# Optimization experiments

Hardware: AMD Instinct MI355X
Metric: run time of the kernel (lower is better)

The kernel has to match this reference:

```python
import jax, jax.numpy as jnp
import numpy as np

LRELU_SLOPE = 0.2  # PyG GATConv default negative_slope
LN_EPS = 1e-5


def _layer_norm(x, g, b):
    mu = x.mean(-1, keepdims=True)
    var = x.var(-1, keepdims=True)
    return (x - mu) / jnp.sqrt(var + LN_EPS) * g + b


def _gat_conv(x, src, dst, W, a_src, a_dst, bias, heads, out_c, concat):
    # PyG GATConv (eval mode, self-loops already appended to src/dst).
    N = x.shape[0]
    h = (x @ W).reshape(N, heads, out_c)            # [N,H,C]
    e_src = (h * a_src).sum(-1)                     # [N,H]
    e_dst = (h * a_dst).sum(-1)                     # [N,H]
    e = jax.nn.leaky_relu(e_src[src] + e_dst[dst], LRELU_SLOPE)  # [E,H]
    # segment softmax over incoming edges of each dst node
    m = jax.ops.segment_max(e, dst, num_segments=N)
    m = jnp.where(jnp.isfinite(m), m, 0.0)
    w = jnp.exp(e - m[dst])
    denom = jax.ops.segment_sum(w, dst, num_segments=N)
    alpha = w / (denom[dst] + 1e-16)                # [E,H]
    out = jax.ops.segment_sum(h[src] * alpha[:, :, None], dst, num_segments=N)  # [N,H,C]
    out = out.reshape(N, heads * out_c) if concat else out.mean(1)
    return out + bias


def setup_inputs() -> dict:
    key = jax.random.key(0)
    ks = jax.random.split(key, 16)
    N, E, F0, Hd, H, G = 50000, 800000, 32, 32, 4, 512
    s = 0.1
    nrm = lambda k, shape: jax.random.normal(k, shape, jnp.float32) * s
    d = {}
    d['x'] = jax.random.normal(ks[0], (N, F0), jnp.float32)
    d['edge_index'] = jax.random.randint(ks[1], (2, E), 0, N)
    d['batch'] = jnp.sort(jax.random.randint(ks[2], (N,), 0, G))
    d['num_graphs'] = G
    # layer 1: F0 -> (Hd, H heads, concat)
    d['W1'] = nrm(ks[3], (F0, H * Hd)); d['as1'] = nrm(ks[4], (H, Hd)); d['ad1'] = nrm(ks[5], (H, Hd))
    d['b1'] = jnp.zeros((H * Hd,)); d['g1'] = jnp.ones((H * Hd,)); d['be1'] = jnp.zeros((H * Hd,))
    # layer 2: H*Hd -> (Hd, H heads, concat)
    d['W2'] = nrm(ks[6], (H * Hd, H * Hd)); d['as2'] = nrm(ks[7], (H, Hd)); d['ad2'] = nrm(ks[8], (H, Hd))
    d['b2'] = jnp.zeros((H * Hd,)); d['g2'] = jnp.ones((H * Hd,)); d['be2'] = jnp.zeros((H * Hd,))
    # layer 3: H*Hd -> (Hd, 1 head, mean)
    d['W3'] = nrm(ks[9], (H * Hd, Hd)); d['as3'] = nrm(ks[10], (1, Hd)); d['ad3'] = nrm(ks[11], (1, Hd))
    d['b3'] = jnp.zeros((Hd,)); d['g3'] = jnp.ones((Hd,)); d['be3'] = jnp.zeros((Hd,))
    # classifier MLP: 2*Hd -> Hd -> Hd//2 -> 1 (torch Linear [out,in])
    d['cW1'] = nrm(ks[12], (Hd, 2 * Hd)); d['cb1'] = jnp.zeros((Hd,))
    d['cW2'] = nrm(ks[13], (Hd // 2, Hd)); d['cb2'] = jnp.zeros((Hd // 2,))
    d['cW3'] = nrm(ks[14], (1, Hd // 2)); d['cb3'] = jnp.zeros((1,))
    return d


def reference(x, edge_index, batch, num_graphs,
              W1, as1, ad1, b1, g1, be1,
              W2, as2, ad2, b2, g2, be2,
              W3, as3, ad3, b3, g3, be3,
              cW1, cb1, cW2, cb2, cW3, cb3):
    N = x.shape[0]
    loop = jnp.arange(N)
    src = jnp.concatenate([edge_index[0], loop])
    dst = jnp.concatenate([edge_index[1], loop])
    h = jax.nn.elu(_layer_norm(_gat_conv(x, src, dst, W1, as1, ad1, b1, 4, 32, True), g1, be1))
    h = jax.nn.elu(_layer_norm(_gat_conv(h, src, dst, W2, as2, ad2, b2, 4, 32, True), g2, be2))
    h = jax.nn.elu(_layer_norm(_gat_conv(h, src, dst, W3, as3, ad3, b3, 1, 32, False), g3, be3))
    cnt = jax.ops.segment_sum(jnp.ones((N,), h.dtype), batch, num_segments=num_graphs)
    x_mean = jax.ops.segment_sum(h, batch, num_segments=num_graphs) / jnp.maximum(cnt, 1.0)[:, None]
    x_max = jax.ops.segment_max(h, batch, num_segments=num_graphs)
    f = jnp.concatenate([x_mean, x_max], axis=1)        # [G, 64]
    f = jax.nn.relu(f @ cW1.T + cb1)
    f = jax.nn.relu(f @ cW2.T + cb2)
    return (f @ cW3.T + cb3).squeeze(-1)                 # [G]
```

## Files before the change

kernel.cpp:

```cpp
#include <hip/hip_runtime.h>
#include <hip/hip_fp16.h>
#include <math.h>

#define CDIV(a, b) (((a) + (b) - 1) / (b))
#define SCAN_BS 1024
#define NBUK 512
#define ATILE 4096

typedef _Float16 f16x8 __attribute__((ext_vector_type(8)));
typedef float f32x4 __attribute__((ext_vector_type(4)));

__device__ __forceinline__ unsigned encf(float v) {
    unsigned u = __float_as_uint(v);
    return (u & 0x80000000u) ? ~u : (u | 0x80000000u);
}
__device__ __forceinline__ float decf(unsigned k) {
    unsigned u = (k & 0x80000000u) ? (k ^ 0x80000000u) : ~k;
    return __uint_as_float(u);
}

__device__ __forceinline__ float lrelu(float v) {
    return v > 0.f ? v : 0.2f * v;
}

__global__ __launch_bounds__(256) void gemm_kernel(
    const float* __restrict__ X, const float* __restrict__ W,
    float* __restrict__ Y, int M, int K, int Nout) {
    int idx = blockIdx.x * blockDim.x + threadIdx.x;
    if (idx >= M * Nout) return;
    int row = idx / Nout;
    int col = idx - row * Nout;
    const float* xr = X + (size_t)row * K;
    const float* wc = W + col;
    float acc = 0.f;
    for (int k = 0; k < K; k += 4) {
        float4 xv = *(const float4*)(xr + k);
        acc += xv.x * wc[(size_t)(k + 0) * Nout];
        acc += xv.y * wc[(size_t)(k + 1) * Nout];
        acc += xv.z * wc[(size_t)(k + 2) * Nout];
        acc += xv.w * wc[(size_t)(k + 3) * Nout];
    }
    Y[idx] = acc;
}

__device__ __forceinline__ void wprep_one(const float* __restrict__ W,
                                          __half* __restrict__ Whf, int K,
                                          int NOUT, int idx) {
    int NK = K / 32;
    int l = idx & 63, f = idx >> 6;
    int ks = f % NK, tt = f / NK;
    int quad = l >> 4, c15 = l & 15;
    _Float16 v[8];
#pragma unroll
    for (int j = 0; j < 8; ++j) {
        int k = ks * 32 + quad * 8 + j;
        int n = tt * 16 + c15;
        v[j] = (_Float16)W[(size_t)k * NOUT + n];
    }
    *(uint4*)(Whf + (size_t)idx * 8) = *(uint4*)v;
}

__global__ __launch_bounds__(256) void wprep_all_kernel(
    const float* __restrict__ W1, const float* __restrict__ W2,
    const float* __restrict__ W3, __half* __restrict__ wh1,
    __half* __restrict__ wh2, __half* __restrict__ wh3,
    int* __restrict__ rowptr, int N, int E) {
    int idx = blockIdx.x * 256 + threadIdx.x;
    if (idx == 0) rowptr[N] = E + N;
    if (idx < 512) {
        wprep_one(W1, wh1, 32, 128, idx);
    } else if (idx < 2560) {
        wprep_one(W2, wh2, 128, 128, idx - 512);
    } else if (idx < 3072) {
        wprep_one(W3, wh3, 128, 32, idx - 2560);
    }
}

__device__ __forceinline__ f16x8 loadA(const float* p) {
    float4 lo = *(const float4*)p;
    float4 hi = *(const float4*)(p + 4);
    f16x8 a;
    a[0] = (_Float16)lo.x; a[1] = (_Float16)lo.y;
    a[2] = (_Float16)lo.z; a[3] = (_Float16)lo.w;
    a[4] = (_Float16)hi.x; a[5] = (_Float16)hi.y;
    a[6] = (_Float16)hi.z; a[7] = (_Float16)hi.w;
    return a;
}
__device__ __forceinline__ f16x8 loadA(const __half* p) {
    return *(const f16x8*)p;
}

template <int K, int NOUT, int HH, typename XT>
__global__ __launch_bounds__(256) void gemm_mfma_attn(
    const XT* __restrict__ X, const __half* __restrict__ Whf,
    __half* __restrict__ Y, const float* __restrict__ a_src,
    const float* __restrict__ a_dst, float* __restrict__ es,
    float* __restrict__ ed, int M) {
    constexpr int NK = K / 32, NT = NOUT / 16;
    static_assert(NT == 2 * HH, "32 channels per head assumed");
    int wave = threadIdx.x >> 6, lane = threadIdx.x & 63;
    int quad = lane >> 4, c15 = lane & 15;
    int row0 = (blockIdx.x * 4 + wave) * 16;
    if (row0 >= M) return;
    int arow = row0 + c15;
    if (arow >= M) arow = M - 1;
    const XT* xr = X + (size_t)arow * K + quad * 8;
    const f16x8* bp = (const f16x8*)Whf;
    f32x4 acc[NT];
#pragma unroll
    for (int t = 0; t < NT; ++t) {
        acc[t][0] = 0.f; acc[t][1] = 0.f; acc[t][2] = 0.f; acc[t][3] = 0.f;
    }
#pragma unroll
    for (int ks = 0; ks < NK; ++ks) {
        f16x8 a = loadA(xr + ks * 32);
#pragma unroll
        for (int t = 0; t < NT; ++t) {
            f16x8 b = bp[(t * NK + ks) * 64 + lane];
            acc[t] = __builtin_amdgcn_mfma_f32_16x16x32_f16(a, b, acc[t],
                                                            0, 0, 0);
        }
    }
#pragma unroll
    for (int r = 0; r < 4; ++r) {
        int row = row0 + quad * 4 + r;
        if (row < M) {
#pragma unroll
            for (int t = 0; t < NT; ++t)
                Y[(size_t)row * NOUT + t * 16 + c15] = (__half)acc[t][r];
        }
    }
    float asv[NT], adv[NT];
#pragma unroll
    for (int t = 0; t < NT; ++t) {
        asv[t] = a_src[t * 16 + c15];
        adv[t] = a_dst[t * 16 + c15];
    }
#pragma unroll
    for (int h = 0; h < HH; ++h) {
#pragma unroll
        for (int r = 0; r < 4; ++r) {
            float s = acc[2 * h][r] * asv[2 * h] +
                      acc[2 * h + 1][r] * asv[2 * h + 1];
            float dd = acc[2 * h][r] * adv[2 * h] +
                       acc[2 * h + 1][r] * adv[2 * h + 1];
#pragma unroll
            for (int off = 8; off >= 1; off >>= 1) {
                s += __shfl_xor(s, off);
                dd += __shfl_xor(dd, off);
            }
            int row = row0 + quad * 4 + r;
            if (row < M) {
                if (c15 == 0) es[row * HH + h] = s;
                if (c15 == 1) ed[row * HH + h] = dd;
            }
        }
    }
}

__global__ __launch_bounds__(256) void binA1_kernel(
    const int* __restrict__ ei, int E, int* __restrict__ ghist,
    int* __restrict__ pool0, int poolN) {
    __shared__ int lh[NBUK];
    int t = threadIdx.x;
    int gid = blockIdx.x * 256 + t;
    if (gid < poolN) pool0[gid] = 0;
    for (int i = t; i < NBUK; i += 256) lh[i] = 0;
    __syncthreads();
    int base = blockIdx.x * ATILE;
#pragma unroll 4
    for (int j = 0; j < ATILE / 256; ++j) {
        int idx = base + t + 256 * j;
        if (idx < E) atomicAdd(&lh[ei[E + idx] >> 7], 1);
    }
    __syncthreads();
    int* gh = ghist + (size_t)blockIdx.x * NBUK;
    for (int i = t; i < NBUK; i += 256) gh[i] = lh[i];
}

__global__ __launch_bounds__(64) void binA2a_kernel(
    int* __restrict__ ghist, int* __restrict__ tot, int nblk) {
    int b = blockIdx.x;
    int lane = threadIdx.x;
    int accb = 0;
    for (int chunk = 0; chunk < nblk; chunk += 64) {
        int i = chunk + lane;
        int v = (i < nblk) ? ghist[(size_t)i * NBUK + b] : 0;
        int s = v;
        for (int off = 1; off < 64; off <<= 1) {
            int tv = __shfl_up(s, off);
            if (lane >= off) s += tv;
        }
        if (i < nblk) ghist[(size_t)i * NBUK + b] = s - v + accb;
        accb += __shfl(s, 63);
    }
    if (lane == 0) tot[b] = accb;
}

__device__ __forceinline__ void bucketScan(const int* __restrict__ tot,
                                           int* __restrict__ sc, int t,
                                           int& a0, int& a1, int& excl) {
    a0 = tot[2 * t];
    a1 = tot[2 * t + 1];
    int pair = a0 + a1;
    sc[t] = pair;
    __syncthreads();
#pragma unroll
    for (int off = 1; off < 256; off <<= 1) {
        int v = (t >= off) ? sc[t - off] : 0;
        __syncthreads();
        sc[t] += v;
        __syncthreads();
    }
    excl = sc[t] - pair;
}

__global__ __launch_bounds__(256) void binA3_kernel(
    const int* __restrict__ ei, int E, const int* __restrict__ ghist,
    const int* __restrict__ tot, unsigned* __restrict__ ebuf) {
    __shared__ int lcur[NBUK];
    __shared__ int sc[256];
    int t = threadIdx.x;
    int a0, a1, excl;
    bucketScan(tot, sc, t, a0, a1, excl);
    const int* gh = ghist + (size_t)blockIdx.x * NBUK;
    lcur[2 * t] = gh[2 * t] + excl;
    lcur[2 * t + 1] = gh[2 * t + 1] + excl + a0;
    __syncthreads();
    int base = blockIdx.x * ATILE;
#pragma unroll 4
    for (int j = 0; j < ATILE / 256; ++j) {
        int idx = base + t + 256 * j;
        if (idx < E) {
            int s = ei[idx];
            int d = ei[E + idx];
            int pos = atomicAdd(&lcur[d >> 7], 1);
            ebuf[pos] = ((unsigned)d << 16) | (unsigned)s;
        }
    }
}

__global__ __launch_bounds__(256) void binB_kernel(
    const unsigned* __restrict__ ebuf, const int* __restrict__ tot,
    int* __restrict__ rowptr, int* __restrict__ csrc, int N) {
    __shared__ int cnt_[128];
    __shared__ int pre[128];
    __shared__ int lcur[128];
    __shared__ int sc[256];
    __shared__ int begS;
    int b = blockIdx.x;
    int t = threadIdx.x;
    int n0 = b << 7;
    int totb = tot[b];
    if (t < 128) cnt_[t] = 0;
    int a0, a1, excl;
    bucketScan(tot, sc, t, a0, a1, excl);
    if (t == (b >> 1)) begS = (b & 1) ? (excl + a0) : excl;
    __syncthreads();
    int beg = begS, end = begS + totb;
    for (int i = beg + t; i < end; i += 256)
        atomicAdd(&cnt_[(ebuf[i] >> 16) - n0], 1);
    __syncthreads();
    if (t < 128) pre[t] = (n0 + t < N) ? (cnt_[t] + 1) : 0;
    __syncthreads();
    for (int off = 1; off < 128; off <<= 1) {
        int v = 0;
        if (t < 128 && t >= off) v = pre[t - off];
        __syncthreads();
        if (t < 128) pre[t] += v;
        __syncthreads();
    }
    int cbase = beg + n0;
    if (t < 128 && n0 + t < N) {
        int ex = pre[t] - (cnt_[t] + 1);
        int rp = cbase + ex;
        rowptr[n0 + t] = rp;
        csrc[rp] = n0 + t;
        lcur[t] = rp + 1;
    }
    __syncthreads();
    for (int i = beg + t; i < end; i += 256) {
        unsigned e = ebuf[i];
        int d = (int)(e >> 16) - n0;
        int s = (int)(e & 0xFFFFu);
        int pos = atomicAdd(&lcur[d], 1);
        csrc[pos] = s;
    }
}

__global__ __launch_bounds__(256) void attn_kernel(
    const float* __restrict__ h, const float* __restrict__ a_src,
    const float* __restrict__ a_dst, float* __restrict__ es,
    float* __restrict__ ed, int N, int H, int C) {
    int idx = blockIdx.x * blockDim.x + threadIdx.x;
    if (idx >= N * H) return;
    int n = idx / H;
    int hh = idx - n * H;
    const float* hp = h + (size_t)n * H * C + (size_t)hh * C;
    const float* ap = a_src + hh * C;
    const float* bp = a_dst + hh * C;
    float s = 0.f, d = 0.f;
    for (int c = 0; c < C; c += 4) {
        float4 hv = *(const float4*)(hp + c);
        float4 av = *(const float4*)(ap + c);
        float4 bv = *(const float4*)(bp + c);
        s += hv.x * av.x + hv.y * av.y + hv.z * av.z + hv.w * av.w;
        d += hv.x * bv.x + hv.y * bv.y + hv.z * bv.z + hv.w * bv.w;
    }
    es[idx] = s;
    ed[idx] = d;
}

__global__ __launch_bounds__(256) void deg_kernel(const int* __restrict__ ei,
                                                  int E,
                                                  int* __restrict__ deg) {
    int e = blockIdx.x * blockDim.x + threadIdx.x;
    if (e >= E) return;
    atomicAdd(&deg[ei[E + e]], 1);
}

__global__ __launch_bounds__(SCAN_BS) void scan1_kernel(
    const int* __restrict__ deg, int* __restrict__ rowptr,
    int* __restrict__ bsum, int N) {
    __shared__ int tmp[SCAN_BS];
    int tid = threadIdx.x;
    int gid = blockIdx.x * SCAN_BS + tid;
    int v = (gid < N) ? (deg[gid] + 1) : 0;
    tmp[tid] = v;
    __syncthreads();
    for (int off = 1; off < SCAN_BS; off <<= 1) {
        int t = (tid >= off) ? tmp[tid - off] : 0;
        __syncthreads();
        tmp[tid] += t;
        __syncthreads();
    }
    if (gid < N) rowptr[gid] = tmp[tid] - v;
    if (tid == SCAN_BS - 1) bsum[blockIdx.x] = tmp[tid];
}

__global__ void scan2_kernel(int* __restrict__ bsum, int nb) {
    if (threadIdx.x == 0 && blockIdx.x == 0) {
        int acc = 0;
        for (int i = 0; i < nb; ++i) {
            int t = bsum[i];
            bsum[i] = acc;
            acc += t;
        }
    }
}

__global__ __launch_bounds__(SCAN_BS) void scan3_kernel(
    int* __restrict__ rowptr, int* __restrict__ cursor,
    int* __restrict__ csrc, const int* __restrict__ bsum, int N, int total) {
    int gid = blockIdx.x * SCAN_BS + threadIdx.x;
    if (gid < N) {
        int v = rowptr[gid] + bsum[blockIdx.x];
        rowptr[gid] = v;
        cursor[gid] = v + 1;
        csrc[v] = gid;
    }
    if (gid == 0) rowptr[N] = total;
}

__global__ __launch_bounds__(256) void scatter_kernel(
    const int* __restrict__ ei, int E, int* __restrict__ cursor,
    int* __restrict__ csrc) {
    int e = blockIdx.x * blockDim.x + threadIdx.x;
    if (e >= E) return;
    int s = ei[e];
    int d = ei[E + e];
    int pos = atomicAdd(&cursor[d], 1);
    csrc[pos] = s;
}

__global__ __launch_bounds__(256) void aggr_ln128_kernel(
    const int* __restrict__ rowptr, const int* __restrict__ csrc,
    const __half* __restrict__ h, const float* __restrict__ es,
    const float* __restrict__ ed, const float* __restrict__ bias,
    const float* __restrict__ gam, const float* __restrict__ bet,
    __half* __restrict__ outp, int N) {
    constexpr int D = 128, H = 4;
    int wave = (blockIdx.x * blockDim.x + threadIdx.x) >> 6;
    int lane = threadIdx.x & 63;
    int grp = lane >> 5;
    int li = lane & 31;
    int d = wave * 2 + grp;
    if (d >= N) return;
    int c = li * 4;
    int hh = li >> 3;
    float edv = ed[d * H + hh];
    float l = 0.f;
    float ax = 0.f, ay = 0.f, az = 0.f, aw = 0.f;
    int k = rowptr[d], end = rowptr[d + 1];
    for (; k + 8 <= end; k += 8) {
        int s[8];
#pragma unroll
        for (int j = 0; j < 8; ++j) s[j] = csrc[k + j];
        float e[8];
#pragma unroll
        for (int j = 0; j < 8; ++j) e[j] = es[s[j] * H + hh];
        uint2 u[8];
#pragma unroll
        for (int j = 0; j < 8; ++j)
            u[j] = *(const uint2*)(h + (size_t)s[j] * D + c);
#pragma unroll
        for (int j = 0; j < 8; ++j) {
            float w = __expf(lrelu(e[j] + edv));
            float2 f0 = __half22float2(*(__half2*)&u[j].x);
            float2 f1 = __half22float2(*(__half2*)&u[j].y);
            l += w;
            ax += w * f0.x; ay += w * f0.y; az += w * f1.x; aw += w * f1.y;
        }
    }
    for (; k + 4 <= end; k += 4) {
        int s[4];
#pragma unroll
        for (int j = 0; j < 4; ++j) s[j] = csrc[k + j];
        float e[4];
#pragma unroll
        for (int j = 0; j < 4; ++j) e[j] = es[s[j] * H + hh];
        uint2 u[4];
#pragma unroll
        for (int j = 0; j < 4; ++j)
            u[j] = *(const uint2*)(h + (size_t)s[j] * D + c);
#pragma unroll
        for (int j = 0; j < 4; ++j) {
            float w = __expf(lrelu(e[j] + edv));
            float2 f0 = __half22float2(*(__half2*)&u[j].x);
            float2 f1 = __half22float2(*(__half2*)&u[j].y);
            l += w;
            ax += w * f0.x; ay += w * f0.y; az += w * f1.x; aw += w * f1.y;
        }
    }
    for (; k < end; ++k) {
        int s = csrc[k];
        float w = __expf(lrelu(es[s * H + hh] + edv));
        uint2 u = *(const uint2*)(h + (size_t)s * D + c);
        float2 f0 = __half22float2(*(__half2*)&u.x);
        float2 f1 = __half22float2(*(__half2*)&u.y);
        l += w;
        ax += w * f0.x; ay += w * f0.y; az += w * f1.x; aw += w * f1.y;
    }
    float rl = 1.f / (l + 1e-16f);
    float4 b4 = *(const float4*)(bias + c);
    float v0 = ax * rl + b4.x;
    float v1 = ay * rl + b4.y;
    float v2 = az * rl + b4.z;
    float v3 = aw * rl + b4.w;
    float s = v0 + v1 + v2 + v3;
    float ss = v0 * v0 + v1 * v1 + v2 * v2 + v3 * v3;
    for (int off = 16; off; off >>= 1) {
        s += __shfl_xor(s, off);
        ss += __shfl_xor(ss, off);
    }
    float mean = s / D;
    float var = ss / D - mean * mean;
    float rstd = rsqrtf(var + 1e-5f);
    float4 g4 = *(const float4*)(gam + c);
    float4 t4 = *(const float4*)(bet + c);
    float4 o;
    o.x = (v0 - mean) * rstd * g4.x + t4.x;
    o.y = (v1 - mean) * rstd * g4.y + t4.y;
    o.z = (v2 - mean) * rstd * g4.z + t4.z;
    o.w = (v3 - mean) * rstd * g4.w + t4.w;
    o.x = o.x > 0.f ? o.x : expm1f(o.x);
    o.y = o.y > 0.f ? o.y : expm1f(o.y);
    o.z = o.z > 0.f ? o.z : expm1f(o.z);
    o.w = o.w > 0.f ? o.w : expm1f(o.w);
    __half2 p0 = __floats2half2_rn(o.x, o.y);
    __half2 p1 = __floats2half2_rn(o.z, o.w);
    uint2 u;
    u.x = *(unsigned*)&p0;
    u.y = *(unsigned*)&p1;
    *(uint2*)(outp + (size_t)d * D + c) = u;
}

__global__ __launch_bounds__(256) void aggr_ln32_pool_kernel(
    const int* __restrict__ rowptr, const int* __restrict__ csrc,
    const __half* __restrict__ h, const float* __restrict__ es,
    const float* __restrict__ ed, const float* __restrict__ bias,
    const float* __restrict__ gam, const float* __restrict__ bet,
    const int* __restrict__ batch, float* __restrict__ psum,
    unsigned* __restrict__ pmax, float* __restrict__ cnt, int N) {
    constexpr int D = 32;
    __shared__ float lsum[2][32];
    __shared__ unsigned lmax[2][32];
    __shared__ float lcnt[2];
    __shared__ int g0s;
    int tid = threadIdx.x;
    int wave = (blockIdx.x * blockDim.x + tid) >> 6;
    int lane = tid & 63;
    int half = lane >> 5;
    int c = lane & 31;
    int d = wave * 2 + half;
    int dbase = blockIdx.x * 8;
    if (tid < 64) {
        lsum[tid >> 5][tid & 31] = 0.f;
        lmax[tid >> 5][tid & 31] = 0u;
    }
    if (tid < 2) lcnt[tid] = 0.f;
    if (tid == 0) g0s = batch[dbase < N ? dbase : (N - 1)];
    __syncthreads();
    int g0 = g0s;
    bool active = d < N;
    if (active) {
        float edv = ed[d];
        float l = 0.f, acc = 0.f;
        int k = rowptr[d], end = rowptr[d + 1];
        for (; k + 8 <= end; k += 8) {
            int s[8];
#pragma unroll
            for (int j = 0; j < 8; ++j) s[j] = csrc[k + j];
            float e[8];
#pragma unroll
            for (int j = 0; j < 8; ++j) e[j] = es[s[j]];
            float hv[8];
#pragma unroll
            for (int j = 0; j < 8; ++j)
                hv[j] = __half2float(h[(size_t)s[j] * D + c]);
#pragma unroll
            for (int j = 0; j < 8; ++j) {
                float w = __expf(lrelu(e[j] + edv));
                l += w;
                acc += w * hv[j];
            }
        }
        for (; k + 4 <= end; k += 4) {
            int s[4];
#pragma unroll
            for (int j = 0; j < 4; ++j) s[j] = csrc[k + j];
            float e[4];
#pragma unroll
            for (int j = 0; j < 4; ++j) e[j] = es[s[j]];
            float hv[4];
#pragma unroll
            for (int j = 0; j < 4; ++j)
                hv[j] = __half2float(h[(size_t)s[j] * D + c]);
#pragma unroll
            for (int j = 0; j < 4; ++j) {
                float w = __expf(lrelu(e[j] + edv));
                l += w;
                acc += w * hv[j];
            }
        }
        for (; k < end; ++k) {
            int s = csrc[k];
            float w = __expf(lrelu(es[s] + edv));
            l += w;
            acc += w * __half2float(h[(size_t)s * D + c]);
        }
        float v = acc / (l + 1e-16f) + bias[c];
        float sm = v, ss = v * v;
        for (int off = 16; off; off >>= 1) {
            sm += __shfl_xor(sm, off);
            ss += __shfl_xor(ss, off);
        }
        float mean = sm / D;
        float var = ss / D - mean * mean;
        float rstd = rsqrtf(var + 1e-5f);
        float o = (v - mean) * rstd * gam[c] + bet[c];
        o = o > 0.f ? o : expm1f(o);
        int g = batch[d];
        int goff = g - g0;
        if (goff >= 0 && goff < 2) {
            atomicAdd(&lsum[goff][c], o);
            atomicMax(&lmax[goff][c], encf(o));
            if (c == 0) atomicAdd(&lcnt[goff], 1.0f);
        } else {
            atomicAdd(&psum[g * D + c], o);
            atomicMax(&pmax[g * D + c], encf(o));
            if (c == 0) atomicAdd(&cnt[g], 1.0f);
        }
    }
    __syncthreads();
    if (tid < 64) {
        int go = tid >> 5, cc = tid & 31;
        unsigned m = lmax[go][cc];
        if (m != 0u) {
            int gg = g0 + go;
            atomicAdd(&psum[gg * D + cc], lsum[go][cc]);
            atomicMax(&pmax[gg * D + cc], m);
            if (cc == 0) atomicAdd(&cnt[gg], lcnt[go]);
        }
    }
}

__global__ __launch_bounds__(256) void aggr_csr_kernel(
    const int* __restrict__ rowptr, const int* __restrict__ csrc,
    const float* __restrict__ h, const float* __restrict__ es,
    const float* __restrict__ ed, float* __restrict__ outp, int N, int H,
    int C) {
    int D = H * C;
    int wave = (blockIdx.x * blockDim.x + threadIdx.x) >> 6;
    int lane = threadIdx.x & 63;
    if (wave >= N) return;
    int d = wave;
    int c0 = lane, c1 = lane + 64;
    bool a0 = c0 < D, a1 = c1 < D;
    int h0 = a0 ? c0 / C : 0;
    int h1 = a1 ? c1 / C : 0;
    float edv0 = a0 ? ed[d * H + h0] : 0.f;
    float edv1 = a1 ? ed[d * H + h1] : 0.f;
    float m0 = -INFINITY, m1 = -INFINITY;
    float l0 = 0.f, l1 = 0.f, acc0 = 0.f, acc1 = 0.f;
    int beg = rowptr[d], end = rowptr[d + 1];
    for (int k = beg; k < end; ++k) {
        int s = csrc[k];
        const float* hp = h + (size_t)s * D;
        if (a0) {
            float v = lrelu(es[s * H + h0] + edv0);
            float nm = fmaxf(m0, v);
            float sc = __expf(m0 - nm);
            float w = __expf(v - nm);
            l0 = l0 * sc + w;
            acc0 = acc0 * sc + w * hp[c0];
            m0 = nm;
        }
        if (a1) {
            float v = lrelu(es[s * H + h1] + edv1);
            float nm = fmaxf(m1, v);
            float sc = __expf(m1 - nm);
            float w = __expf(v - nm);
            l1 = l1 * sc + w;
            acc1 = acc1 * sc + w * hp[c1];
            m1 = nm;
        }
    }
    if (a0) outp[(size_t)d * D + c0] = acc0 / (l0 + 1e-16f);
    if (a1) outp[(size_t)d * D + c1] = acc1 / (l1 + 1e-16f);
}

__global__ __launch_bounds__(64) void ln_elu_kernel(
    const float* __restrict__ in, const float* __restrict__ bias,
    const float* __restrict__ gam, const float* __restrict__ bet,
    float* __restrict__ outp, int D) {
    int n = blockIdx.x;
    int lane = threadIdx.x;
    int c0 = lane, c1 = lane + 64;
    bool a0 = c0 < D, a1 = c1 < D;
    float v0 = 0.f, v1 = 0.f;
    if (a0) v0 = in[(size_t)n * D + c0] + bias[c0];
    if (a1) v1 = in[(size_t)n * D + c1] + bias[c1];
    float s = v0 + v1;
    float ss = v0 * v0 + v1 * v1;
    for (int off = 32; off; off >>= 1) {
        s += __shfl_xor(s, off);
        ss += __shfl_xor(ss, off);
    }
    float mean = s / D;
    float var = ss / D - mean * mean;
    float rstd = rsqrtf(var + 1e-5f);
    if (a0) {
        float o = (v0 - mean) * rstd * gam[c0] + bet[c0];
        outp[(size_t)n * D + c0] = o > 0.f ? o : expm1f(o);
    }
    if (a1) {
        float o = (v1 - mean) * rstd * gam[c1] + bet[c1];
        outp[(size_t)n * D + c1] = o > 0.f ? o : expm1f(o);
    }
}

__global__ __launch_bounds__(256) void pool_kernel(
    const float* __restrict__ h, const int* __restrict__ batch, int N, int C,
    float* __restrict__ psum, unsigned* __restrict__ pmax,
    float* __restrict__ cnt) {
    int idx = blockIdx.x * blockDim.x + threadIdx.x;
    if (idx >= N * C) return;
    int n = idx / C;
    int c = idx - n * C;
    int g = batch[n];
    float v = h[(size_t)n * C + c];
    atomicAdd(&psum[g * C + c], v);
    atomicMax(&pmax[g * C + c], encf(v));
    if (c == 0) atomicAdd(&cnt[g], 1.0f);
}

__global__ __launch_bounds__(64) void mlp_kernel(
    const float* __restrict__ psum, const unsigned* __restrict__ pmax,
    const float* __restrict__ cnt, const float* __restrict__ cW1,
    const float* __restrict__ cb1, const float* __restrict__ cW2,
    const float* __restrict__ cb2, const float* __restrict__ cW3,
    const float* __restrict__ cb3, float* __restrict__ outp, int C) {
    __shared__ float f[64];
    __shared__ float t1[32];
    __shared__ float t2[16];
    int g = blockIdx.x;
    int t = threadIdx.x;
    float c = fmaxf(cnt[g], 1.0f);
    if (t < C) {
        f[t] = psum[g * C + t] / c;
    } else if (t < 2 * C) {
        unsigned k = pmax[g * C + (t - C)];
        f[t] = (k == 0u) ? -INFINITY : decf(k);
    }
    __syncthreads();
    if (t < 32) {
        float a = cb1[t];
        for (int i = 0; i < 64; ++i) a += f[i] * cW1[t * 64 + i];
        t1[t] = fmaxf(a, 0.f);
    }
    __syncthreads();
    if (t < 16) {
        float a = cb2[t];
        for (int i = 0; i < 32; ++i) a += t1[i] * cW2[t * 32 + i];
        t2[t] = fmaxf(a, 0.f);
    }
    __syncthreads();
    if (t == 0) {
        float a = cb3[0];
        for (int i = 0; i < 16; ++i) a += t2[i] * cW3[i];
        outp[g] = a;
    }
}

extern "C" void kernel_launch(void* const* d_in, const int* in_sizes, int n_in,
                              void* d_out, int out_size, void* d_ws,
                              size_t ws_size, hipStream_t stream) {
    const float* x = (const float*)d_in[0];
    const int* ei = (const int*)d_in[1];
    const int* batch = (const int*)d_in[2];
    const float* W1 = (const float*)d_in[4];
    const float* as1 = (const float*)d_in[5];
    const float* ad1 = (const float*)d_in[6];
    const float* b1 = (const float*)d_in[7];
    const float* g1 = (const float*)d_in[8];
    const float* be1 = (const float*)d_in[9];
    const float* W2 = (const float*)d_in[10];
    const float* as2 = (const float*)d_in[11];
    const float* ad2 = (const float*)d_in[12];
    const float* b2 = (const float*)d_in[13];
    const float* g2 = (const float*)d_in[14];
    const float* be2 = (const float*)d_in[15];
    const float* W3 = (const float*)d_in[16];
    const float* as3 = (const float*)d_in[17];
    const float* ad3 = (const float*)d_in[18];
    const float* b3 = (const float*)d_in[19];
    const float* g3 = (const float*)d_in[20];
    const float* be3 = (const float*)d_in[21];
    const float* cW1 = (const float*)d_in[22];
    const float* cb1 = (const float*)d_in[23];
    const float* cW2 = (const float*)d_in[24];
    const float* cb2 = (const float*)d_in[25];
    const float* cW3 = (const float*)d_in[26];
    const float* cb3 = (const float*)d_in[27];

    const int N = in_sizes[2];
    const int E = in_sizes[1] / 2;
    const int F0 = in_sizes[0] / N;
    const int Hd = in_sizes[19];
    const int H = in_sizes[5] / Hd;
    const int D = H * Hd;
    const int H3 = in_sizes[17] / Hd;
    const int G = out_size;
    const int EN = E + N;
    const bool shapes_ok = (F0 == 32 && Hd == 32 && H == 4 && D == 128 &&
                            H3 == 1 && N <= 65536);

    char* w = (char*)d_ws;
    size_t off = 0;
    auto carve = [&](size_t bytes) -> void* {
        void* p = w + off;
        off = (off + bytes + 255) & ~(size_t)255;
        return p;
    };
    float* Q = (float*)carve((size_t)N * D * 4);
    __half* Qh = (__half*)Q;
    float* R = (float*)carve((size_t)N * D * 4);
    float* P = (float*)carve((size_t)N * D * 4);
    __half* Ph = (__half*)P;
    float* es = (float*)carve((size_t)N * H * 4);
    float* ed = (float*)carve((size_t)N * H * 4);
    int* rowptr = (int*)carve((size_t)(N + 1) * 4);
    int* cursor = (int*)carve((size_t)N * 4);
    int* csrc = (int*)carve((size_t)EN * 4);
    int* bsum = (int*)carve((size_t)CDIV(N, SCAN_BS) * 4);
    const int nblkA = CDIV(E, ATILE);
    int* ghist = (int*)carve((size_t)nblkA * NBUK * 4);
    int* tot = (int*)carve((size_t)NBUK * 4);
    unsigned* ebuf = (unsigned*)carve((size_t)E * 4);
    __half* wh1 = (__half*)carve((size_t)8 * 1 * 64 * 8 * 2);
    __half* wh2 = (__half*)carve((size_t)8 * 4 * 64 * 8 * 2);
    __half* wh3 = (__half*)carve((size_t)2 * 4 * 64 * 8 * 2);
    float* psum = (float*)carve((size_t)G * Hd * 4);
    unsigned* pmax = (unsigned*)carve((size_t)G * Hd * 4);
    float* cnt = (float*)carve((size_t)G * 4);
    (void)ws_size;
    (void)n_in;

    const int BLK = 256;
    const int nb = CDIV(N, SCAN_BS);
    const int poolInts = G * Hd * 2 + G;

    if (shapes_ok) {
        binA1_kernel<<<nblkA, 256, 0, stream>>>(ei, E, ghist, (int*)psum,
                                                poolInts);
        binA2a_kernel<<<NBUK, 64, 0, stream>>>(ghist, tot, nblkA);
        binA3_kernel<<<nblkA, 256, 0, stream>>>(ei, E, ghist, tot, ebuf);
        binB_kernel<<<CDIV(N, 128), 256, 0, stream>>>(ebuf, tot, rowptr,
                                                      csrc, N);
        wprep_all_kernel<<<12, 256, 0, stream>>>(W1, W2, W3, wh1, wh2, wh3,
                                                 rowptr, N, E);
        gemm_mfma_attn<32, 128, 4, float><<<CDIV(N, 64), 256, 0, stream>>>(
            x, wh1, Qh, as1, ad1, es, ed, N);
        aggr_ln128_kernel<<<CDIV(N, 8), 256, 0, stream>>>(
            rowptr, csrc, Qh, es, ed, b1, g1, be1, Ph, N);
        gemm_mfma_attn<128, 128, 4, __half><<<CDIV(N, 64), 256, 0, stream>>>(
            Ph, wh2, Qh, as2, ad2, es, ed, N);
        aggr_ln128_kernel<<<CDIV(N, 8), 256, 0, stream>>>(
            rowptr, csrc, Qh, es, ed, b2, g2, be2, Ph, N);
        gemm_mfma_attn<128, 32, 1, __half><<<CDIV(N, 64), 256, 0, stream>>>(
            Ph, wh3, Qh, as3, ad3, es, ed, N);
        aggr_ln32_pool_kernel<<<CDIV(N, 8), 256, 0, stream>>>(
            rowptr, csrc, Qh, es, ed, b3, g3, be3, batch, psum, pmax, cnt, N);
    } else {
        hipMemsetAsync(psum, 0, (size_t)G * Hd * 4, stream);
        hipMemsetAsync(pmax, 0, (size_t)G * Hd * 4, stream);
        hipMemsetAsync(cnt, 0, (size_t)G * 4, stream);
        hipMemsetAsync(cursor, 0, (size_t)N * 4, stream);
        deg_kernel<<<CDIV(E, BLK), BLK, 0, stream>>>(ei, E, cursor);
        scan1_kernel<<<nb, SCAN_BS, 0, stream>>>(cursor, rowptr, bsum, N);
        scan2_kernel<<<1, 64, 0, stream>>>(bsum, nb);
        scan3_kernel<<<nb, SCAN_BS, 0, stream>>>(rowptr, cursor, csrc, bsum, N, EN);
        scatter_kernel<<<CDIV(E, BLK), BLK, 0, stream>>>(ei, E, cursor, csrc);
        gemm_kernel<<<CDIV(N * D, BLK), BLK, 0, stream>>>(x, W1, Q, N, F0, D);
        attn_kernel<<<CDIV(N * H, BLK), BLK, 0, stream>>>(Q, as1, ad1, es, ed, N, H, Hd);
        aggr_csr_kernel<<<CDIV(N, 4), BLK, 0, stream>>>(rowptr, csrc, Q, es, ed, R, N, H, Hd);
        ln_elu_kernel<<<N, 64, 0, stream>>>(R, b1, g1, be1, P, D);
        gemm_kernel<<<CDIV(N * D, BLK), BLK, 0, stream>>>(P, W2, Q, N, D, D);
        attn_kernel<<<CDIV(N * H, BLK), BLK, 0, stream>>>(Q, as2, ad2, es, ed, N, H, Hd);
        aggr_csr_kernel<<<CDIV(N, 4), BLK, 0, stream>>>(rowptr, csrc, Q, es, ed, R, N, H, Hd);
        ln_elu_kernel<<<N, 64, 0, stream>>>(R, b2, g2, be2, P, D);
        gemm_kernel<<<CDIV(N * Hd, BLK), BLK, 0, stream>>>(P, W3, Q, N, D, Hd);
        attn_kernel<<<CDIV(N * H3, BLK), BLK, 0, stream>>>(Q, as3, ad3, es, ed, N, H3, Hd);
        aggr_csr_kernel<<<CDIV(N, 4), BLK, 0, stream>>>(rowptr, csrc, Q, es, ed, R, N, H3, Hd);
        ln_elu_kernel<<<N, 64, 0, stream>>>(R, b3, g3, be3, P, Hd);
        pool_kernel<<<CDIV(N * Hd, BLK), BLK, 0, stream>>>(P, batch, N, Hd, psum, pmax, cnt);
    }

    mlp_kernel<<<G, 64, 0, stream>>>(psum, pmax, cnt, cW1, cb1, cW2, cb2, cW3,
                                     cb3, (float*)d_out, Hd);
}
```

Before: 295.4 us.

## Assign one wavefront per destination node and split edges across lane subgroups

The GAT aggregation kernels now map one 64-lane wavefront to each destination node instead of two nodes per wave. Lanes are split into subgroups that each process a different incoming edge: four groups of 16 lanes with 16-byte loads for the 128-wide layers, and eight groups of 8 lanes with 8-byte loads for the 32-wide layer. Partial sums are combined with cross-lane shuffles. The aim is more memory-level parallelism per node and wider gathers, at the cost of extra shuffle reductions, idle lanes during the LayerNorm/ELU epilogue, and twice as many blocks.

```diff
diff --git a/kernel.cpp b/kernel.cpp
--- a/kernel.cpp
+++ b/kernel.cpp
@@ -380,99 +380,109 @@
     const float* __restrict__ gam, const float* __restrict__ bet,
     __half* __restrict__ outp, int N) {
     constexpr int D = 128, H = 4;
-    int wave = (blockIdx.x * blockDim.x + threadIdx.x) >> 6;
+    int d = (blockIdx.x * blockDim.x + threadIdx.x) >> 6;
     int lane = threadIdx.x & 63;
-    int grp = lane >> 5;
-    int li = lane & 31;
-    int d = wave * 2 + grp;
     if (d >= N) return;
-    int c = li * 4;
-    int hh = li >> 3;
+    int sub = lane >> 4;
+    int cl = lane & 15;
+    int c = cl * 8;
+    int hh = cl >> 2;
     float edv = ed[d * H + hh];
+    float acc[8];
+#pragma unroll
+    for (int i = 0; i < 8; ++i) acc[i] = 0.f;
     float l = 0.f;
-    float ax = 0.f, ay = 0.f, az = 0.f, aw = 0.f;
-    int k = rowptr[d], end = rowptr[d + 1];
-    for (; k + 8 <= end; k += 8) {
-        int s[8];
-#pragma unroll
-        for (int j = 0; j < 8; ++j) s[j] = csrc[k + j];
-        float e[8];
-#pragma unroll
-        for (int j = 0; j < 8; ++j) e[j] = es[s[j] * H + hh];
-        uint2 u[8];
-#pragma unroll
-        for (int j = 0; j < 8; ++j)
-            u[j] = *(const uint2*)(h + (size_t)s[j] * D + c);
-#pragma unroll
-        for (int j = 0; j < 8; ++j) {
-            float w = __expf(lrelu(e[j] + edv));
-            float2 f0 = __half22float2(*(__half2*)&u[j].x);
-            float2 f1 = __half22float2(*(__half2*)&u[j].y);
+    int beg = rowptr[d], end = rowptr[d + 1];
+    int k = beg;
+    for (; k + 16 <= end; k += 16) {
+        int s[4];
+#pragma unroll
+        for (int r = 0; r < 4; ++r) s[r] = csrc[k + 4 * r + sub];
+        float e[4];
+#pragma unroll
+        for (int r = 0; r < 4; ++r) e[r] = es[s[r] * H + hh];
+        uint4 u[4];
+#pragma unroll
+        for (int r = 0; r < 4; ++r)
+            u[r] = *(const uint4*)(h + (size_t)s[r] * D + c);
+#pragma unroll
+        for (int r = 0; r < 4; ++r) {
+            float w = __expf(lrelu(e[r] + edv));
             l += w;
-            ax += w * f0.x; ay += w * f0.y; az += w * f1.x; aw += w * f1.y;
-        }
-    }
-    for (; k + 4 <= end; k += 4) {
-        int s[4];
-#pragma unroll
-        for (int j = 0; j < 4; ++j) s[j] = csrc[k + j];
-        float e[4];
-#pragma unroll
-        for (int j = 0; j < 4; ++j) e[j] = es[s[j] * H + hh];
-        uint2 u[4];
-#pragma unroll
-        for (int j = 0; j < 4; ++j)
-            u[j] = *(const uint2*)(h + (size_t)s[j] * D + c);
-#pragma unroll
-        for (int j = 0; j < 4; ++j) {
-            float w = __expf(lrelu(e[j] + edv));
-            float2 f0 = __half22float2(*(__half2*)&u[j].x);
-            float2 f1 = __half22float2(*(__half2*)&u[j].y);
-            l += w;
-            ax += w * f0.x; ay += w * f0.y; az += w * f1.x; aw += w * f1.y;
-        }
-    }
-    for (; k < end; ++k) {
-        int s = csrc[k];
-        float w = __expf(lrelu(es[s * H + hh] + edv));
-        uint2 u = *(const uint2*)(h + (size_t)s * D + c);
-        float2 f0 = __half22float2(*(__half2*)&u.x);
-        float2 f1 = __half22float2(*(__half2*)&u.y);
+            const __half2* hp = (const __half2*)&u[r];
+#pragma unroll
+            for (int i = 0; i < 4; ++i) {
+                float2 f = __half22float2(hp[i]);
+                acc[2 * i] += w * f.x;
+                acc[2 * i + 1] += w * f.y;
+            }
+        }
+    }
+    for (; k < end; k += 4) {
+        int slot = k + sub;
+        bool ok = slot < end;
+        int s = csrc[ok ? slot : beg];
+        float e = es[s * H + hh];
+        uint4 u = *(const uint4*)(h + (size_t)s * D + c);
+        float w = ok ? __expf(lrelu(e + edv)) : 0.f;
         l += w;
-        ax += w * f0.x; ay += w * f0.y; az += w * f1.x; aw += w * f1.y;
-    }
+        const __half2* hp = (const __half2*)&u;
+#pragma unroll
+        for (int i = 0; i < 4; ++i) {
+            float2 f = __half22float2(hp[i]);
+            acc[2 * i] += w * f.x;
+            acc[2 * i + 1] += w * f.y;
+        }
+    }
+#pragma unroll
+    for (int i = 0; i < 8; ++i) acc[i] += __shfl_xor(acc[i], 16);
+    l += __shfl_xor(l, 16);
+#pragma unroll
+    for (int i = 0; i < 8; ++i) acc[i] += __shfl_xor(acc[i], 32);
+    l += __shfl_xor(l, 32);
     float rl = 1.f / (l + 1e-16f);
-    float4 b4 = *(const float4*)(bias + c);
-    float v0 = ax * rl + b4.x;
-    float v1 = ay * rl + b4.y;
-    float v2 = az * rl + b4.z;
-    float v3 = aw * rl + b4.w;
-    float s = v0 + v1 + v2 + v3;
-    float ss = v0 * v0 + v1 * v1 + v2 * v2 + v3 * v3;
-    for (int off = 16; off; off >>= 1) {
-        s += __shfl_xor(s, off);
-        ss += __shfl_xor(ss, off);
-    }
-    float mean = s / D;
-    float var = ss / D - mean * mean;
+    float4 b0 = *(const float4*)(bias + c);
+    float4 b1 = *(const float4*)(bias + c + 4);
+    float v[8];
+    v[0] = acc[0] * rl + b0.x; v[1] = acc[1] * rl + b0.y;
+    v[2] = acc[2] * rl + b0.z; v[3] = acc[3] * rl + b0.w;
+    v[4] = acc[4] * rl + b1.x; v[5] = acc[5] * rl + b1.y;
+    v[6] = acc[6] * rl + b1.z; v[7] = acc[7] * rl + b1.w;
+    float sm = 0.f, ssum = 0.f;
+#pragma unroll
+    for (int i = 0; i < 8; ++i) { sm += v[i]; ssum += v[i] * v[i]; }
+#pragma unroll
+    for (int off = 1; off <= 8; off <<= 1) {
+        sm += __shfl_xor(sm, off);
+        ssum += __shfl_xor(ssum, off);
+    }
+    float mean = sm / D;
+    float var = ssum / D - mean * mean;
     float rstd = rsqrtf(var + 1e-5f);
-    float4 g4 = *(const float4*)(gam + c);
-    float4 t4 = *(const float4*)(bet + c);
-    float4 o;
-    o.x = (v0 - mean) * rstd * g4.x + t4.x;
-    o.y = (v1 - mean) * rstd * g4.y + t4.y;
-    o.z = (v2 - mean) * rstd * g4.z + t4.z;
-    o.w = (v3 - mean) * rstd * g4.w + t4.w;
-    o.x = o.x > 0.f ? o.x : expm1f(o.x);
-    o.y = o.y > 0.f ? o.y : expm1f(o.y);
-    o.z = o.z > 0.f ? o.z : expm1f(o.z);
-    o.w = o.w > 0.f ? o.w : expm1f(o.w);
-    __half2 p0 = __floats2half2_rn(o.x, o.y);
-    __half2 p1 = __floats2half2_rn(o.z, o.w);
-    uint2 u;
-    u.x = *(unsigned*)&p0;
-    u.y = *(unsigned*)&p1;
-    *(uint2*)(outp + (size_t)d * D + c) = u;
+    if (sub == 0) {
+        float4 g0 = *(const float4*)(gam + c);
+        float4 g1 = *(const float4*)(gam + c + 4);
+        float4 t0 = *(const float4*)(bet + c);
+        float4 t1 = *(const float4*)(bet + c + 4);
+        float gv[8] = {g0.x, g0.y, g0.z, g0.w, g1.x, g1.y, g1.z, g1.w};
+        float tv[8] = {t0.x, t0.y, t0.z, t0.w, t1.x, t1.y, t1.z, t1.w};
+        __half2 p[4];
+#pragma unroll
+        for (int i = 0; i < 4; ++i) {
+            float o0 = (v[2 * i] - mean) * rstd * gv[2 * i] + tv[2 * i];
+            float o1 = (v[2 * i + 1] - mean) * rstd * gv[2 * i + 1] +
+                       tv[2 * i + 1];
+            o0 = o0 > 0.f ? o0 : expm1f(o0);
+            o1 = o1 > 0.f ? o1 : expm1f(o1);
+            p[i] = __floats2half2_rn(o0, o1);
+        }
+        uint4 uo;
+        uo.x = *(unsigned*)&p[0];
+        uo.y = *(unsigned*)&p[1];
+        uo.z = *(unsigned*)&p[2];
+        uo.w = *(unsigned*)&p[3];
+        *(uint4*)(outp + (size_t)d * D + c) = uo;
+    }
 }
 
 __global__ __launch_bounds__(256) void aggr_ln32_pool_kernel(
@@ -488,12 +498,12 @@
     __shared__ float lcnt[2];
     __shared__ int g0s;
     int tid = threadIdx.x;
-    int wave = (blockIdx.x * blockDim.x + tid) >> 6;
+    int d = (blockIdx.x * blockDim.x + tid) >> 6;
     int lane = tid & 63;
-    int half = lane >> 5;
-    int c = lane & 31;
-    int d = wave * 2 + half;
-    int dbase = blockIdx.x * 8;
+    int sub = lane >> 3;
+    int cl = lane & 7;
+    int c = cl * 4;
+    int dbase = blockIdx.x * 4;
     if (tid < 64) {
         lsum[tid >> 5][tid & 31] = 0.f;
         lmax[tid >> 5][tid & 31] = 0u;
@@ -505,71 +515,100 @@
     bool active = d < N;
     if (active) {
         float edv = ed[d];
-        float l = 0.f, acc = 0.f;
-        int k = rowptr[d], end = rowptr[d + 1];
-        for (; k + 8 <= end; k += 8) {
-            int s[8];
-#pragma unroll
-            for (int j = 0; j < 8; ++j) s[j] = csrc[k + j];
-            float e[8];
-#pragma unroll
-            for (int j = 0; j < 8; ++j) e[j] = es[s[j]];
-            float hv[8];
-#pragma unroll
-            for (int j = 0; j < 8; ++j)
-                hv[j] = __half2float(h[(size_t)s[j] * D + c]);
-#pragma unroll
-            for (int j = 0; j < 8; ++j) {
-                float w = __expf(lrelu(e[j] + edv));
+        float acc[4] = {0.f, 0.f, 0.f, 0.f};
+        float l = 0.f;
+        int beg = rowptr[d], end = rowptr[d + 1];
+        int k = beg;
+        for (; k + 16 <= end; k += 16) {
+            int s[2];
+#pragma unroll
+            for (int r = 0; r < 2; ++r) s[r] = csrc[k + 8 * r + sub];
+            float e[2];
+#pragma unroll
+            for (int r = 0; r < 2; ++r) e[r] = es[s[r]];
+            uint2 u[2];
+#pragma unroll
+            for (int r = 0; r < 2; ++r)
+                u[r] = *(const uint2*)(h + (size_t)s[r] * D + c);
+#pragma unroll
+            for (int r = 0; r < 2; ++r) {
+                float w = __expf(lrelu(e[r] + edv));
                 l += w;
-                acc += w * hv[j];
+                float2 f0 = __half22float2(*(__half2*)&u[r].x);
+                float2 f1 = __half22float2(*(__half2*)&u[r].y);
+                acc[0] += w * f0.x; acc[1] += w * f0.y;
+                acc[2] += w * f1.x; acc[3] += w * f1.y;
             }
         }
-        for (; k + 4 <= end; k += 4) {
-            int s[4];
-#pragma unroll
-            for (int j = 0; j < 4; ++j) s[j] = csrc[k + j];
-            float e[4];
-#pragma unroll
-            for (int j = 0; j < 4; ++j) e[j] = es[s[j]];
-            float hv[4];
-#pragma unroll
-            for (int j = 0; j < 4; ++j)
-                hv[j] = __half2float(h[(size_t)s[j] * D + c]);
-#pragma unroll
-            for (int j = 0; j < 4; ++j) {
-                float w = __expf(lrelu(e[j] + edv));
-                l += w;
-                acc += w * hv[j];
+        for (; k < end; k += 8) {
+            int slot = k + sub;
+            bool ok = slot < end;
+            int s = csrc[ok ? slot : beg];
+            float e = es[s];
+            uint2 u = *(const uint2*)(h + (size_t)s * D + c);
+            float w = ok ? __expf(lrelu(e + edv)) : 0.f;
+            l += w;
+            float2 f0 = __half22float2(*(__half2*)&u.x);
+            float2 f1 = __half22float2(*(__half2*)&u.y);
+            acc[0] += w * f0.x; acc[1] += w * f0.y;
+            acc[2] += w * f1.x; acc[3] += w * f1.y;
+        }
+#pragma unroll
+        for (int off = 8; off <= 32; off <<= 1) {
+#pragma unroll
+            for (int i = 0; i < 4; ++i) acc[i] += __shfl_xor(acc[i], off);
+            l += __shfl_xor(l, off);
+        }
+        float rl = 1.f / (l + 1e-16f);
+        float4 b4 = *(const float4*)(bias + c);
+        float v0 = acc[0] * rl + b4.x;
+        float v1 = acc[1] * rl + b4.y;
+        float v2 = acc[2] * rl + b4.z;
+        float v3 = acc[3] * rl + b4.w;
+        float sm = v0 + v1 + v2 + v3;
+        float ssum = v0 * v0 + v1 * v1 + v2 * v2 + v3 * v3;
+#pragma unroll
+        for (int off = 1; off <= 4; off <<= 1) {
+            sm += __shfl_xor(sm, off);
+            ssum += __shfl_xor(ssum, off);
+        }
+        float mean = sm / D;
+        float var = ssum / D - mean * mean;
+        float rstd = rsqrtf(var + 1e-5f);
+        if (sub == 0) {
+            float4 g4 = *(const float4*)(gam + c);
+            float4 t4 = *(const float4*)(bet + c);
+            float o0 = (v0 - mean) * rstd * g4.x + t4.x;
+            float o1 = (v1 - mean) * rstd * g4.y + t4.y;
+            float o2 = (v2 - mean) * rstd * g4.z + t4.z;
+            float o3 = (v3 - mean) * rstd * g4.w + t4.w;
+            o0 = o0 > 0.f ? o0 : expm1f(o0);
+            o1 = o1 > 0.f ? o1 : expm1f(o1);
+            o2 = o2 > 0.f ? o2 : expm1f(o2);
+            o3 = o3 > 0.f ? o3 : expm1f(o3);
+            int g = batch[d];
+            int goff = g - g0;
+            if (goff >= 0 && goff < 2) {
+                atomicAdd(&lsum[goff][c + 0], o0);
+                atomicAdd(&lsum[goff][c + 1], o1);
+                atomicAdd(&lsum[goff][c + 2], o2);
+                atomicAdd(&lsum[goff][c + 3], o3);
+                atomicMax(&lmax[goff][c + 0], encf(o0));
+                atomicMax(&lmax[goff][c + 1], encf(o1));
+                atomicMax(&lmax[goff][c + 2], encf(o2));
+                atomicMax(&lmax[goff][c + 3], encf(o3));
+                if (lane == 0) atomicAdd(&lcnt[goff], 1.0f);
+            } else {
+                atomicAdd(&psum[g * D + c + 0], o0);
+                atomicAdd(&psum[g * D + c + 1], o1);
+                atomicAdd(&psum[g * D + c + 2], o2);
+                atomicAdd(&psum[g * D + c + 3], o3);
+                atomicMax(&pmax[g * D + c + 0], encf(o0));
+                atomicMax(&pmax[g * D + c + 1], encf(o1));
+                atomicMax(&pmax[g * D + c + 2], encf(o2));
+                atomicMax(&pmax[g * D + c + 3], encf(o3));
+                if (lane == 0) atomicAdd(&cnt[g], 1.0f);
             }
-        }
-        for (; k < end; ++k) {
-            int s = csrc[k];
-            float w = __expf(lrelu(es[s] + edv));
-            l += w;
-            acc += w * __half2float(h[(size_t)s * D + c]);
-        }
-        float v = acc / (l + 1e-16f) + bias[c];
-        float sm = v, ss = v * v;
-        for (int off = 16; off; off >>= 1) {
-            sm += __shfl_xor(sm, off);
-            ss += __shfl_xor(ss, off);
-        }
-        float mean = sm / D;
-        float var = ss / D - mean * mean;
-        float rstd = rsqrtf(var + 1e-5f);
-        float o = (v - mean) * rstd * gam[c] + bet[c];
-        o = o > 0.f ? o : expm1f(o);
-        int g = batch[d];
-        int goff = g - g0;
-        if (goff >= 0 && goff < 2) {
-            atomicAdd(&lsum[goff][c], o);
-            atomicMax(&lmax[goff][c], encf(o));
-            if (c == 0) atomicAdd(&lcnt[goff], 1.0f);
-        } else {
-            atomicAdd(&psum[g * D + c], o);
-            atomicMax(&pmax[g * D + c], encf(o));
-            if (c == 0) atomicAdd(&cnt[g], 1.0f);
         }
     }
     __syncthreads();
@@ -802,15 +841,15 @@
                                                  rowptr, N, E);
         gemm_mfma_attn<32, 128, 4, float><<<CDIV(N, 64), 256, 0, stream>>>(
             x, wh1, Qh, as1, ad1, es, ed, N);
-        aggr_ln128_kernel<<<CDIV(N, 8), 256, 0, stream>>>(
+        aggr_ln128_kernel<<<CDIV(N, 4), 256, 0, stream>>>(
             rowptr, csrc, Qh, es, ed, b1, g1, be1, Ph, N);
         gemm_mfma_attn<128, 128, 4, __half><<<CDIV(N, 64), 256, 0, stream>>>(
             Ph, wh2, Qh, as2, ad2, es, ed, N);
-        aggr_ln128_kernel<<<CDIV(N, 8), 256, 0, stream>>>(
+        aggr_ln128_kernel<<<CDIV(N, 4), 256, 0, stream>>>(
             rowptr, csrc, Qh, es, ed, b2, g2, be2, Ph, N);
         gemm_mfma_attn<128, 32, 1, __half><<<CDIV(N, 64), 256, 0, stream>>>(
             Ph, wh3, Qh, as3, ad3, es, ed, N);
-        aggr_ln32_pool_kernel<<<CDIV(N, 8), 256, 0, stream>>>(
+        aggr_ln32_pool_kernel<<<CDIV(N, 4), 256, 0, stream>>>(
             rowptr, csrc, Qh, es, ed, b3, g3, be3, batch, psum, pmax, cnt, N);
     } else {
         hipMemsetAsync(psum, 0, (size_t)G * Hd * 4, stream);
```

Result: slower. 316.9 us (+7.3%).
